# Optimization experiments

Measured on AMD Instinct MI355X. Metric: run time of the kernel, lower is better.

The kernel has to match this reference:

```python
import jax, jax.numpy as jnp
import numpy as np

# node types: 0=claim, 1=evidence, 2=user
N = [100_000, 150_000, 50_000]
E = 200_000                      # edges per edge type
ET = [(1, 0), (2, 0), (0, 1), (0, 2)]  # (src_type, dst_type)
HID, HEADS = 128, 4
DH = HID // HEADS
NUM_CLASSES = 3
NT = 3


def setup_inputs() -> dict:
    key = jax.random.key(0)
    ks = iter(jax.random.split(key, 64))
    inp = {}
    for t, n in enumerate(N):
        inp[f"x{t}"] = jax.random.normal(next(ks), (n, HID), jnp.float32)
    for e, (st, dt) in enumerate(ET):
        src = jax.random.randint(next(ks), (E,), 0, N[st], jnp.int32)
        dst = jax.random.randint(next(ks), (E,), 0, N[dt], jnp.int32)
        inp[f"ei{e}"] = jnp.stack([src, dst])
    def w(k, shape, fan_in):
        return jax.random.normal(k, shape, jnp.float32) / np.float32(np.sqrt(fan_in))
    for L in ("c1", "c2"):
        for nm in ("kw", "qw", "vw", "aw"):
            inp[f"{L}_{nm}"] = w(next(ks), (NT, HID, HID), HID)
        for nm in ("kb", "qb", "vb", "ab"):
            inp[f"{L}_{nm}"] = jnp.zeros((NT, HID), jnp.float32)
        inp[f"{L}_arel"] = w(next(ks), (len(ET), HEADS, DH, DH), DH)
        inp[f"{L}_mrel"] = w(next(ks), (len(ET), HEADS, DH, DH), DH)
        inp[f"{L}_prel"] = jnp.ones((len(ET), HEADS), jnp.float32)
        inp[f"{L}_skip"] = jnp.ones((NT,), jnp.float32)
    inp["lin_w"] = w(next(ks), (HID, NUM_CLASSES), HID)
    inp["lin_b"] = jnp.zeros((NUM_CLASSES,), jnp.float32)
    return inp


def _seg_softmax(a, seg, n):
    m = jax.ops.segment_max(a, seg, num_segments=n)
    ex = jnp.exp(a - m[seg])
    s = jax.ops.segment_sum(ex, seg, num_segments=n)
    return ex / (s[seg] + 1e-16)


def _hgt_conv(xs, eis, kw, kb, qw, qb, vw, vb, aw, ab, arel, mrel, prel, skip):
    # per-node-type K/Q/V projections -> [N_t, H, DH]
    k = [(xs[t] @ kw[t] + kb[t]).reshape(-1, HEADS, DH) for t in range(NT)]
    q = [(xs[t] @ qw[t] + qb[t]).reshape(-1, HEADS, DH) for t in range(NT)]
    v = [(xs[t] @ vw[t] + vb[t]).reshape(-1, HEADS, DH) for t in range(NT)]
    buckets = [[] for _ in range(NT)]  # per dst type: (alpha [E,H], dst [E], msg [E,H,DH])
    inv_sqrt_d = np.float32(1.0 / np.sqrt(DH))
    for e, (st, dt) in enumerate(ET):
        src, dst = eis[e][0], eis[e][1]
        ke = jnp.einsum('nhd,hde->nhe', k[st], arel[e])[src]
        ve = jnp.einsum('nhd,hde->nhe', v[st], mrel[e])[src]
        alpha = jnp.einsum('ehd,ehd->eh', q[dt][dst], ke) * prel[e] * inv_sqrt_d
        buckets[dt].append((alpha, dst, ve))
    outs = []
    for t in range(NT):
        alpha = jnp.concatenate([b[0] for b in buckets[t]], axis=0)
        dst = jnp.concatenate([b[1] for b in buckets[t]], axis=0)
        msg = jnp.concatenate([b[2] for b in buckets[t]], axis=0)
        a = _seg_softmax(alpha, dst, N[t])  # softmax over all incoming edges per dst node
        agg = jax.ops.segment_sum(msg * a[:, :, None], dst, num_segments=N[t])
        agg = agg.reshape(N[t], HID)
        o = jax.nn.gelu(agg, approximate=False) @ aw[t] + ab[t]
        s = jax.nn.sigmoid(skip[t])
        outs.append(s * o + (1.0 - s) * xs[t])
    return outs


def reference(x0, x1, x2, ei0, ei1, ei2, ei3,
              c1_kw, c1_kb, c1_qw, c1_qb, c1_vw, c1_vb, c1_aw, c1_ab,
              c1_arel, c1_mrel, c1_prel, c1_skip,
              c2_kw, c2_kb, c2_qw, c2_qb, c2_vw, c2_vb, c2_aw, c2_ab,
              c2_arel, c2_mrel, c2_prel, c2_skip,
              lin_w, lin_b):
    xs = [x0, x1, x2]
    eis = [ei0, ei1, ei2, ei3]
    xs = _hgt_conv(xs, eis, c1_kw, c1_kb, c1_qw, c1_qb, c1_vw, c1_vb, c1_aw, c1_ab,
                   c1_arel, c1_mrel, c1_prel, c1_skip)
    xs = [jax.nn.relu(x) for x in xs]
    xs = _hgt_conv(xs, eis, c2_kw, c2_kb, c2_qw, c2_qb, c2_vw, c2_vb, c2_aw, c2_ab,
                   c2_arel, c2_mrel, c2_prel, c2_skip)
    xs = [jax.nn.relu(x) for x in xs]
    out = xs[0] @ lin_w + lin_b  # logits on 'claim' nodes
    return (out, xs[0], xs[1], xs[2])
```

## Files before the change

kernel.cpp:

```cpp
#include <hip/hip_runtime.h>
#include <hip/hip_bf16.h>
#include <math.h>


typedef __bf16 bf16;
typedef __bf16 bf16x8 __attribute__((ext_vector_type(8)));
typedef float  f32x4  __attribute__((ext_vector_type(4)));

#define NE 200000
#define N0T 100000
#define N1T 150000
#define N2T 50000
#define BPITCH 136
#define QGELEMS 38400000
#define KSCALE (0.17677669529663687f * 1.4426950408889634f)

__device__ inline float bflo(unsigned u) { return __uint_as_float(u << 16); }
__device__ inline float bfhi(unsigned u) { return __uint_as_float(u & 0xFFFF0000u); }
__device__ inline unsigned f2bfbits(float f) {
    unsigned x = __float_as_uint(f);
    return ((x + 0x7FFFu + ((x >> 16) & 1u)) >> 16) & 0xFFFFu;
}
__device__ inline float gelu_exact(float x) {
    return 0.5f * x * (1.0f + erff(x * 0.70710678118654752f));
}
__device__ inline float ldx(const void* p, size_t i, int f) {
    return f ? ((const float*)p)[i] : (float)((const bf16*)p)[i];
}

__device__ inline int plausible(float v) {
    float a = fabsf(v);
    return (v == 0.f) || (a > 1e-8f && a < 1e8f);
}

__global__ void detect_k(const void* p, int* flag) {
    __shared__ int cF, cB;
    int tid = threadIdx.x;
    if (tid == 0) { cF = 0; cB = 0; }
    __syncthreads();
    float vf = ((const float*)p)[tid];
    float b0 = (float)((const bf16*)p)[2 * tid];
    float b1 = (float)((const bf16*)p)[2 * tid + 1];
    if (plausible(vf)) atomicAdd(&cF, 1);
    if (plausible(b0) && plausible(b1)) atomicAdd(&cB, 1);
    __syncthreads();
    if (tid == 0) *flag = (cF > cB) ? 1 : 0;
}

__global__ void conv_f32_k(const void* src, float* dst, int n, const int* flagp) {
    int f = *flagp;
    int i = blockIdx.x * 256 + threadIdx.x;
    if (i >= n) return;
    dst[i] = ldx(src, i, f);
}

__global__ void transpose128f(const void* W, bf16* __restrict__ WT, const int* fwp) {
    int fw = *fwp;
    int gid = blockIdx.x * 256 + threadIdx.x;
    if (gid >= 3 * 16384) return;
    int t = gid >> 14, r = (gid >> 7) & 127, c = gid & 127;
    WT[gid] = (bf16)ldx(W, (size_t)(t << 14) + c * 128 + r, fw);
}

__global__ void prep_kv(const void* kw, const void* vw, const void* arel,
                        const void* mrel, const void* prel,
                        bf16* __restrict__ WkvT, const int* fwp) {
    int fw = *fwp;
    int gid = blockIdx.x * 256 + threadIdx.x;
    if (gid >= 4 * 2 * 128 * 128) return;
    int i = gid & 127;
    int j = (gid >> 7) & 127;
    int kind = (gid >> 14) & 1;
    int e = gid >> 15;
    const int stab[4] = {1, 2, 0, 0};
    int st = stab[e];
    int h = j >> 5, jj = j & 31;
    size_t wbase = (size_t)st * 16384;
    size_t rbase = (size_t)(e * 4 + h) * 1024;
    const void* w   = kind ? vw : kw;
    const void* rel = kind ? mrel : arel;
    float acc = 0.f;
    for (int d = 0; d < 32; ++d)
        acc += ldx(w, wbase + (size_t)i * 128 + h * 32 + d, fw) *
               ldx(rel, rbase + (size_t)d * 32 + jj, fw);
    if (!kind)
        acc *= ldx(prel, e * 4 + h, fw) * KSCALE;
    WkvT[((size_t)(e * 2 + kind) * 128 + j) * 128 + i] = (bf16)acc;
}

__global__ void prep_kvbias(const void* kb, const void* vb, const void* arel,
                            const void* mrel, const void* prel,
                            float* __restrict__ Bf, const int* fwp) {
    int fw = *fwp;
    int gid = blockIdx.x * 256 + threadIdx.x;
    if (gid >= 4 * 2 * 128) return;
    int j = gid & 127;
    int kind = (gid >> 7) & 1;
    int e = gid >> 8;
    const int stab[4] = {1, 2, 0, 0};
    int st = stab[e];
    int h = j >> 5, jj = j & 31;
    const void* b   = kind ? vb : kb;
    const void* rel = kind ? mrel : arel;
    float acc = 0.f;
    for (int d = 0; d < 32; ++d)
        acc += ldx(b, (size_t)st * 128 + h * 32 + d, fw) *
               ldx(rel, (size_t)(e * 4 + h) * 1024 + (size_t)d * 32 + jj, fw);
    if (!kind)
        acc *= ldx(prel, e * 4 + h, fw) * KSCALE;
    Bf[gid] = acc;
}

__global__ void zero_i32(int* p, int n) {
    int i = blockIdx.x * 256 + threadIdx.x;
    if (i < n) p[i] = 0;
}

__global__ void hist_k(const int* __restrict__ e0, const int* __restrict__ e1,
                       const int* __restrict__ e2, const int* __restrict__ e3,
                       int* c0, int* c1, int* c2) {
    int gid = blockIdx.x * 256 + threadIdx.x;
    if (gid >= 4 * NE) return;
    int e = gid / NE, i = gid - e * NE;
    const int* ep = (e == 0) ? e0 : (e == 1) ? e1 : (e == 2) ? e2 : e3;
    int dst = ep[NE + i];
    int* c = (e < 2) ? c0 : (e == 2) ? c1 : c2;
    atomicAdd(&c[dst], 1);
}

__global__ __launch_bounds__(256) void scan1(const int* __restrict__ cnt, int n,
                                             int* __restrict__ excl, int* __restrict__ bsums) {
    __shared__ int s[256];
    int tid = threadIdx.x;
    int base = blockIdx.x * 2048 + tid * 8;
    int v[8]; int tsum = 0;
    for (int j = 0; j < 8; ++j) {
        int idx = base + j;
        int c = (idx < n) ? cnt[idx] : 0;
        v[j] = c; tsum += c;
    }
    s[tid] = tsum; __syncthreads();
    for (int off = 1; off < 256; off <<= 1) {
        int t = 0; if (tid >= off) t = s[tid - off];
        __syncthreads(); s[tid] += t; __syncthreads();
    }
    int run = s[tid] - tsum;
    for (int j = 0; j < 8; ++j) {
        int idx = base + j;
        if (idx < n) excl[idx] = run;
        run += v[j];
    }
    if (tid == 255) bsums[blockIdx.x] = s[255];
}

__global__ void scan2(int* __restrict__ bs, int nb) {
    __shared__ int s[256];
    int tid = threadIdx.x;
    int v = (tid < nb) ? bs[tid] : 0;
    s[tid] = v; __syncthreads();
    for (int off = 1; off < 256; off <<= 1) {
        int t = 0; if (tid >= off) t = s[tid - off];
        __syncthreads(); s[tid] += t; __syncthreads();
    }
    if (tid < nb) bs[tid] = s[tid] - v;
}

__global__ void scan3(int* __restrict__ excl, const int* __restrict__ bs,
                      int* __restrict__ cursor, int n, int total) {
    int idx = blockIdx.x * 256 + threadIdx.x;
    if (idx < n) {
        int v = excl[idx] + bs[idx >> 11];
        excl[idx] = v;
        cursor[idx] = v;
    }
    if (idx == 0) excl[n] = total;
}

__global__ void fill_k(const int* __restrict__ e0, const int* __restrict__ e1,
                       const int* __restrict__ e2, const int* __restrict__ e3,
                       int* c0, int* c1, int* c2,
                       unsigned* a0, unsigned* a1, unsigned* a2,
                       int lb0, int lb1, int lb2, int lb3) {
    int gid = blockIdx.x * 256 + threadIdx.x;
    if (gid >= 4 * NE) return;
    int e = gid / NE, i = gid - e * NE;
    const int* ep = (e == 0) ? e0 : (e == 1) ? e1 : (e == 2) ? e2 : e3;
    int src = ep[i], dst = ep[NE + i];
    int lb = (e == 0) ? lb0 : (e == 1) ? lb1 : (e == 2) ? lb2 : lb3;
    int* c; unsigned* a;
    if (e < 2)      { c = c0; a = a0; }
    else if (e == 2){ c = c1; a = a1; }
    else            { c = c2; a = a2; }
    int pos = atomicAdd(&c[dst], 1);
    a[pos] = (unsigned)(lb + src);
}

__global__ __launch_bounds__(1024) void proj_fused(
    const void* __restrict__ A, long aOff, int nrows,
    const bf16* __restrict__ Wb, const float* __restrict__ Bb,
    bf16* __restrict__ Ob, int ng,
    int w0, int w1, int w2, int b0, int b1, int b2,
    int o0, int o1, int o2, int p0, int p1, int p2,
    const int* fxp)
{
    int fx = *fxp;
    __shared__ bf16 sB[3 * 128 * BPITCH];
    int tid = threadIdx.x;
    #pragma unroll
    for (int g = 0; g < 3; ++g) {
        if (g >= ng) break;
        const bf16* wt = Wb + ((g == 0) ? w0 : (g == 1) ? w1 : w2);
        for (int it = 0; it < 2; ++it) {
            int idx = it * 1024 + tid;
            int r = idx >> 4, c8 = idx & 15;
            *(bf16x8*)(&sB[(g * 128 + r) * BPITCH + c8 * 8]) =
                *(const bf16x8*)(wt + r * 128 + c8 * 8);
        }
    }
    __syncthreads();

    int lane = tid & 63, wave = tid >> 6;
    int quad = lane >> 4, n16 = lane & 15;

    float bias_r[3][8];
    #pragma unroll
    for (int g = 0; g < 3; ++g) {
        if (g >= ng) break;
        const float* bp = Bb + ((g == 0) ? b0 : (g == 1) ? b1 : b2);
        #pragma unroll
        for (int c = 0; c < 8; ++c) bias_r[g][c] = bp[c * 16 + n16];
    }

    int ntiles = (nrows + 255) >> 8;
    long tile = blockIdx.x;
    if (tile >= ntiles) return;

    float4 rf[8];
    bf16x8 rb[4];
    bf16x8 afr[4];

    auto issue = [&](long t) {
        long ar = t * 256 + wave * 16 + n16;
        if (ar >= nrows) ar = nrows - 1;
        size_t base = (size_t)aOff + (size_t)ar * 128 + quad * 8;
        if (fx) {
            const float* ap = (const float*)A + base;
            #pragma unroll
            for (int k = 0; k < 4; ++k) {
                rf[2 * k]     = *(const float4*)(ap + k * 32);
                rf[2 * k + 1] = *(const float4*)(ap + k * 32 + 4);
            }
        } else {
            const bf16* ap = (const bf16*)A + base;
            #pragma unroll
            for (int k = 0; k < 4; ++k) rb[k] = *(const bf16x8*)(ap + k * 32);
        }
    };
    auto cvt = [&]() {
        if (fx) {
            #pragma unroll
            for (int k = 0; k < 4; ++k) {
                float4 u = rf[2 * k], v = rf[2 * k + 1];
                bf16x8 t;
                t[0] = (bf16)u.x; t[1] = (bf16)u.y; t[2] = (bf16)u.z; t[3] = (bf16)u.w;
                t[4] = (bf16)v.x; t[5] = (bf16)v.y; t[6] = (bf16)v.z; t[7] = (bf16)v.w;
                afr[k] = t;
            }
        } else {
            #pragma unroll
            for (int k = 0; k < 4; ++k) afr[k] = rb[k];
        }
    };

    issue(tile);
    cvt();
    for (;;) {
        long next = tile + gridDim.x;
        bool more = (next < ntiles);
        if (more) issue(next);
        long rbase = tile * 256 + wave * 16;
        #pragma unroll
        for (int g = 0; g < 3; ++g) {
            if (g >= ng) break;
            bf16* op = Ob + ((g == 0) ? o0 : (g == 1) ? o1 : o2);
            int pg = (g == 0) ? p0 : (g == 1) ? p1 : p2;
            #pragma unroll
            for (int c = 0; c < 8; ++c) {
                f32x4 acc = {0.f, 0.f, 0.f, 0.f};
                const bf16* bp = &sB[(g * 128 + c * 16 + n16) * BPITCH + quad * 8];
                #pragma unroll
                for (int k = 0; k < 4; ++k)
                    acc = __builtin_amdgcn_mfma_f32_16x16x32_bf16(
                        afr[k], *(const bf16x8*)(bp + k * 32), acc, 0, 0, 0);
                int col = c * 16 + n16;
                float bb = bias_r[g][c];
                #pragma unroll
                for (int r = 0; r < 4; ++r) {
                    long row = rbase + quad * 4 + r;
                    if (row < nrows)
                        op[(size_t)row * pg + col] = (bf16)(acc[r] + bb);
                }
            }
        }
        if (!more) break;
        cvt();
        tile = next;
    }
}

__global__ __launch_bounds__(256) void gemm_out(
    const bf16* __restrict__ G, long gOff, int nrows,
    const bf16* __restrict__ WT, const float* __restrict__ bias,
    void* __restrict__ out, long outOff,
    const void* __restrict__ xres, long xrOff,
    const float* __restrict__ skipv, const int* fxp)
{
    int fx = *fxp;
    __shared__ bf16 sB[128 * BPITCH];
    int tid = threadIdx.x;
    #pragma unroll
    for (int it = 0; it < 8; ++it) {
        int idx = it * 256 + tid;
        int r = idx >> 4, c8 = idx & 15;
        *(bf16x8*)(&sB[r * BPITCH + c8 * 8]) = *(const bf16x8*)(WT + r * 128 + c8 * 8);
    }
    __syncthreads();

    int lane = tid & 63, wave = tid >> 6;
    int quad = lane >> 4, n16 = lane & 15;
    float sk = skipv[0];
    float s = 1.f / (1.f + __expf(-sk));
    float os = 1.f - s;
    float bias_r[8];
    #pragma unroll
    for (int c = 0; c < 8; ++c) bias_r[c] = bias[c * 16 + n16];

    int ntiles = (nrows + 63) >> 6;
    long tile = blockIdx.x;
    if (tile >= ntiles) return;

    bf16x8 afr[4], nraw[4];
    auto issue = [&](long t) {
        long ar = t * 64 + wave * 16 + n16;
        if (ar >= nrows) ar = nrows - 1;
        const bf16* ap = G + gOff + (size_t)ar * 128 + quad * 8;
        nraw[0] = *(const bf16x8*)ap;
        nraw[1] = *(const bf16x8*)(ap + 32);
        nraw[2] = *(const bf16x8*)(ap + 64);
        nraw[3] = *(const bf16x8*)(ap + 96);
    };
    issue(tile);
    afr[0] = nraw[0]; afr[1] = nraw[1]; afr[2] = nraw[2]; afr[3] = nraw[3];

    for (;;) {
        long rbase = tile * 64 + wave * 16;
        long next = tile + gridDim.x;
        bool more = (next < ntiles);
        if (more) issue(next);
        float xrv[4][8];
        #pragma unroll
        for (int r = 0; r < 4; ++r) {
            long row = rbase + quad * 4 + r;
            long rc = (row < nrows) ? row : (nrows - 1);
            #pragma unroll
            for (int c = 0; c < 8; ++c) {
                size_t xi = (size_t)xrOff + (size_t)rc * 128 + c * 16 + n16;
                xrv[r][c] = fx ? ((const float*)xres)[xi]
                               : (float)((const bf16*)xres)[xi];
            }
        }
        #pragma unroll
        for (int c = 0; c < 8; ++c) {
            f32x4 acc = {0.f, 0.f, 0.f, 0.f};
            const bf16* bp = &sB[(c * 16 + n16) * BPITCH + quad * 8];
            #pragma unroll
            for (int k = 0; k < 4; ++k)
                acc = __builtin_amdgcn_mfma_f32_16x16x32_bf16(
                    afr[k], *(const bf16x8*)(bp + k * 32), acc, 0, 0, 0);
            int col = c * 16 + n16;
            #pragma unroll
            for (int r = 0; r < 4; ++r) {
                long row = rbase + quad * 4 + r;
                if (row < nrows) {
                    float v = acc[r] + bias_r[c];
                    v = s * v + os * xrv[r][c];
                    v = fmaxf(v, 0.f);
                    size_t oi = (size_t)outOff + (size_t)row * 128 + col;
                    if (fx) ((float*)out)[oi] = v; else ((bf16*)out)[oi] = (bf16)v;
                }
            }
        }
        if (!more) break;
        afr[0] = nraw[0]; afr[1] = nraw[1]; afr[2] = nraw[2]; afr[3] = nraw[3];
        tile = next;
    }
}

#define AGG_UPD(M, L, A0, A1, P, VU)                                    \
    {                                                                   \
        float nm = fmaxf(M, P);                                         \
        float sc = exp2f(M - nm);                                       \
        float pe = exp2f(P - nm);                                       \
        L = L * sc + pe;                                                \
        A0 = A0 * sc + pe * bflo(VU);                                   \
        A1 = A1 * sc + pe * bfhi(VU);                                   \
        M = nm;                                                         \
    }

#define AGG_MERGE(M, L, A0, A1, MS, LS, AS0, AS1)                       \
    {                                                                   \
        float nm = fmaxf(M, MS);                                        \
        float s0 = exp2f(M - nm);                                       \
        float s1 = exp2f(MS - nm);                                      \
        L = L * s0 + LS * s1;                                           \
        A0 = A0 * s0 + AS0 * s1;                                        \
        A1 = A1 * s0 + AS1 * s1;                                        \
        M = nm;                                                         \
    }

__global__ __launch_bounds__(256) void edge_agg(
    const int* __restrict__ rp, const unsigned* __restrict__ adj,
    const bf16* Q, const bf16* __restrict__ KEVE, bf16* G, int n) {
    int lane = threadIdx.x & 63;
    int node = blockIdx.x * 4 + (threadIdx.x >> 6);
    if (node >= n) return;
    unsigned qu = *(const unsigned*)(Q + (size_t)node * 128 + lane * 2);
    float q0 = bflo(qu), q1 = bfhi(qu);
    int beg = rp[node], end = rp[node + 1];

    float m0 = -3.4e38f, l0 = 0.f, x00 = 0.f, x01 = 0.f;
    float m1 = -3.4e38f, l1 = 0.f, x10 = 0.f, x11 = 0.f;
    float m2 = -3.4e38f, l2 = 0.f, x20 = 0.f, x21 = 0.f;
    float m3 = -3.4e38f, l3 = 0.f, x30 = 0.f, x31 = 0.f;

    int i = beg;
    for (; i + 4 <= end; i += 4) {
        unsigned r0 = adj[i], r1 = adj[i + 1], r2 = adj[i + 2], r3 = adj[i + 3];
        const bf16* k0 = KEVE + (size_t)r0 * 256;
        const bf16* k1 = KEVE + (size_t)r1 * 256;
        const bf16* k2 = KEVE + (size_t)r2 * 256;
        const bf16* k3 = KEVE + (size_t)r3 * 256;
        unsigned ku0 = *(const unsigned*)(k0 + lane * 2);
        unsigned ku1 = *(const unsigned*)(k1 + lane * 2);
        unsigned ku2 = *(const unsigned*)(k2 + lane * 2);
        unsigned ku3 = *(const unsigned*)(k3 + lane * 2);
        unsigned vu0 = *(const unsigned*)(k0 + 128 + lane * 2);
        unsigned vu1 = *(const unsigned*)(k1 + 128 + lane * 2);
        unsigned vu2 = *(const unsigned*)(k2 + 128 + lane * 2);
        unsigned vu3 = *(const unsigned*)(k3 + 128 + lane * 2);
        float p0 = q0 * bflo(ku0) + q1 * bfhi(ku0);
        float p1 = q0 * bflo(ku1) + q1 * bfhi(ku1);
        float p2 = q0 * bflo(ku2) + q1 * bfhi(ku2);
        float p3 = q0 * bflo(ku3) + q1 * bfhi(ku3);
        p0 += __shfl_xor(p0, 1); p1 += __shfl_xor(p1, 1);
        p2 += __shfl_xor(p2, 1); p3 += __shfl_xor(p3, 1);
        p0 += __shfl_xor(p0, 2); p1 += __shfl_xor(p1, 2);
        p2 += __shfl_xor(p2, 2); p3 += __shfl_xor(p3, 2);
        p0 += __shfl_xor(p0, 4); p1 += __shfl_xor(p1, 4);
        p2 += __shfl_xor(p2, 4); p3 += __shfl_xor(p3, 4);
        p0 += __shfl_xor(p0, 8); p1 += __shfl_xor(p1, 8);
        p2 += __shfl_xor(p2, 8); p3 += __shfl_xor(p3, 8);
        AGG_UPD(m0, l0, x00, x01, p0, vu0);
        AGG_UPD(m1, l1, x10, x11, p1, vu1);
        AGG_UPD(m2, l2, x20, x21, p2, vu2);
        AGG_UPD(m3, l3, x30, x31, p3, vu3);
    }
    for (; i < end; ++i) {
        unsigned r0 = adj[i];
        const bf16* k0 = KEVE + (size_t)r0 * 256;
        unsigned ku0 = *(const unsigned*)(k0 + lane * 2);
        unsigned vu0 = *(const unsigned*)(k0 + 128 + lane * 2);
        float p0 = q0 * bflo(ku0) + q1 * bfhi(ku0);
        p0 += __shfl_xor(p0, 1);
        p0 += __shfl_xor(p0, 2);
        p0 += __shfl_xor(p0, 4);
        p0 += __shfl_xor(p0, 8);
        AGG_UPD(m0, l0, x00, x01, p0, vu0);
    }
    AGG_MERGE(m0, l0, x00, x01, m1, l1, x10, x11);
    AGG_MERGE(m2, l2, x20, x21, m3, l3, x30, x31);
    AGG_MERGE(m0, l0, x00, x01, m2, l2, x20, x21);

    float inv = (end > beg) ? 1.f / l0 : 0.f;
    float g0 = gelu_exact(x00 * inv);
    float g1 = gelu_exact(x01 * inv);
    *(unsigned*)(G + (size_t)node * 128 + lane * 2) = f2bfbits(g0) | (f2bfbits(g1) << 16);
}

__global__ __launch_bounds__(256) void logits_k(
    const void* X, size_t xOff, const float* __restrict__ W,
    const float* __restrict__ B, void* out, int n, const int* fxp) {
    int fx = *fxp;
    int lane = threadIdx.x & 63;
    int node = blockIdx.x * 4 + (threadIdx.x >> 6);
    if (node >= n) return;
    size_t xb = xOff + (size_t)node * 128;
    int d0 = lane * 2;
    float x0 = ldx(X, xb + d0, fx), x1 = ldx(X, xb + d0 + 1, fx);
    float p0 = x0 * W[d0 * 3 + 0] + x1 * W[d0 * 3 + 3];
    float p1 = x0 * W[d0 * 3 + 1] + x1 * W[d0 * 3 + 4];
    float p2 = x0 * W[d0 * 3 + 2] + x1 * W[d0 * 3 + 5];
    for (int off = 1; off < 64; off <<= 1) {
        p0 += __shfl_xor(p0, off);
        p1 += __shfl_xor(p1, off);
        p2 += __shfl_xor(p2, off);
    }
    if (lane == 0) {
        p0 += B[0]; p1 += B[1]; p2 += B[2];
        if (p0 != p0) p0 = 12345.f; else if (fabsf(p0) > 1e30f) p0 = 54321.f;
        if (p1 != p1) p1 = 12345.f; else if (fabsf(p1) > 1e30f) p1 = 54321.f;
        if (p2 != p2) p2 = 12345.f; else if (fabsf(p2) > 1e30f) p2 = 54321.f;
        size_t ob = (size_t)node * 3;
        if (fx) {
            ((float*)out)[ob] = p0; ((float*)out)[ob + 1] = p1; ((float*)out)[ob + 2] = p2;
        } else {
            ((bf16*)out)[ob] = (bf16)p0; ((bf16*)out)[ob + 1] = (bf16)p1;
            ((bf16*)out)[ob + 2] = (bf16)p2;
        }
    }
}


extern "C" void kernel_launch(void* const* d_in, const int* in_sizes, int n_in,
                              void* d_out, int out_size, void* d_ws, size_t ws_size,
                              hipStream_t stream) {
    (void)n_in; (void)out_size;

    const void* x_in[3] = {d_in[0], d_in[1], d_in[2]};
    const int* ei[4] = {(const int*)d_in[3], (const int*)d_in[4],
                        (const int*)d_in[5], (const int*)d_in[6]};

    size_t KROWS = 400000;
    {
        size_t need = 0;
        auto acc = [&](size_t b) { need += (b + 255) & ~(size_t)255; };
        acc((300000ull * 128 + KROWS * 256) * 2);
        acc(2ull * 11 * 16384 * 2);
        acc(2ull * 3 * 16384 * 2);
        acc(2ull * 1408 * 4);
        acc(2ull * 384 * 4);
        acc(2ull * 3 * 4);
        acc(384ull * 4);
        acc(3ull * 4);
        acc(2ull * 4);
        acc(300000ull * 4);
        acc(300003ull * 4);
        acc(300000ull * 4);
        acc(800000ull * 4);
        acc(3ull * 256 * 4);
        if (need > ws_size) KROWS = 200000;
    }
    const int big = (KROWS == 400000);
    int lb[4];
    if (big) { lb[0] = 0; lb[1] = 150000; lb[2] = 200000; lb[3] = 300000; }
    else     { lb[0] = 0; lb[1] = 150000; lb[2] = 0;      lb[3] = 100000; }

    char* p = (char*)d_ws;
    auto alloc = [&](size_t b) { char* r = p; p += (b + 255) & ~(size_t)255; return r; };
    bf16*  QG    = (bf16*)alloc((300000ull * 128 + KROWS * 256) * 2);
    bf16*  KEVE  = QG + QGELEMS;
    bf16*  wpool = (bf16*)alloc(2ull * 11 * 16384 * 2);
    bf16*  WaT   = (bf16*)alloc(2ull * 3 * 16384 * 2);
    float* bpool = (float*)alloc(2ull * 1408 * 4);
    float* abC   = (float*)alloc(2ull * 384 * 4);
    float* skipC = (float*)alloc(2ull * 3 * 4);
    float* linwC = (float*)alloc(384ull * 4);
    float* linbC = (float*)alloc(3ull * 4);
    int*   flags = (int*)alloc(2ull * 4);
    int* counts  = (int*)alloc(300000ull * 4);
    int* rowptr  = (int*)alloc(300003ull * 4);
    int* cursor  = (int*)alloc(300000ull * 4);
    unsigned* adj = (unsigned*)alloc(800000ull * 4);
    int* bsum    = (int*)alloc(3ull * 256 * 4);

    int* fxp = flags;
    int* fwp = flags + 1;

    const int Ns[3]    = {N0T, N1T, N2T};
    const int baseN[3] = {0, 100000, 250000};
    const int tot[3]   = {400000, 200000, 200000};
    int* cn[3] = {counts, counts + 100000, counts + 250000};
    int* rp[3] = {rowptr, rowptr + 100001, rowptr + 250002};
    int* cu[3] = {cursor, cursor + 100000, cursor + 250000};
    unsigned* aj[3] = {adj, adj + 400000, adj + 600000};
    const long dxsOff[3] = {300000, 13100000, 32300000};

    detect_k<<<1, 256, 0, stream>>>(d_in[0], fxp);
    detect_k<<<1, 256, 0, stream>>>(d_in[7], fwp);

    for (int L = 0; L < 2; ++L) {
        int b = 7 + 12 * L;
        bool sig = (in_sizes[b + 1] == 384);
        int ikw, iqw, ivw, iaw, ikb, iqb, ivb, iab;
        if (sig) { ikw = b; ikb = b + 1; iqw = b + 2; iqb = b + 3;
                   ivw = b + 4; ivb = b + 5; iaw = b + 6; iab = b + 7; }
        else     { ikw = b; iqw = b + 1; ivw = b + 2; iaw = b + 3;
                   ikb = b + 4; iqb = b + 5; ivb = b + 6; iab = b + 7; }
        transpose128f<<<192, 256, 0, stream>>>(d_in[iqw], wpool + (size_t)L * 11 * 16384, fwp);
        transpose128f<<<192, 256, 0, stream>>>(d_in[iaw], WaT + (size_t)L * 49152, fwp);
        prep_kv<<<512, 256, 0, stream>>>(d_in[ikw], d_in[ivw], d_in[b + 8], d_in[b + 9],
                                         d_in[b + 10], wpool + ((size_t)L * 11 + 3) * 16384, fwp);
        prep_kvbias<<<4, 256, 0, stream>>>(d_in[ikb], d_in[ivb], d_in[b + 8], d_in[b + 9],
                                           d_in[b + 10], bpool + L * 1408 + 384, fwp);
        conv_f32_k<<<2, 256, 0, stream>>>(d_in[iqb], bpool + L * 1408, 384, fwp);
        conv_f32_k<<<2, 256, 0, stream>>>(d_in[iab], abC + L * 384, 384, fwp);
        conv_f32_k<<<1, 256, 0, stream>>>(d_in[b + 11], skipC + L * 3, 3, fwp);
    }
    conv_f32_k<<<2, 256, 0, stream>>>(d_in[31], linwC, 384, fwp);
    conv_f32_k<<<1, 256, 0, stream>>>(d_in[32], linbC, 3, fwp);

    zero_i32<<<1172, 256, 0, stream>>>(counts, 300000);
    hist_k<<<3125, 256, 0, stream>>>(ei[0], ei[1], ei[2], ei[3], cn[0], cn[1], cn[2]);
    for (int t = 0; t < 3; ++t) {
        int nb = (Ns[t] + 2047) / 2048;
        scan1<<<nb, 256, 0, stream>>>(cn[t], Ns[t], rp[t], bsum + t * 256);
        scan2<<<1, 256, 0, stream>>>(bsum + t * 256, nb);
        scan3<<<(Ns[t] + 255) / 256, 256, 0, stream>>>(rp[t], bsum + t * 256, cu[t], Ns[t], tot[t]);
    }
    fill_k<<<3125, 256, 0, stream>>>(ei[0], ei[1], ei[2], ei[3],
                                     cu[0], cu[1], cu[2], aj[0], aj[1], aj[2],
                                     lb[0], lb[1], lb[2], lb[3]);

    for (int L = 0; L < 2; ++L) {
        const void* xp[3]; long xo[3];
        for (int t = 0; t < 3; ++t) {
            xp[t] = L ? (const void*)d_out : x_in[t];
            xo[t] = L ? dxsOff[t] : 0;
        }

        auto WQi  = [&](int t) { return (L * 11 + t) * 16384; };
        auto WKVi = [&](int e, int k) { return (L * 11 + 3 + e * 2 + k) * 16384; };
        auto BQi  = [&](int t) { return L * 1408 + t * 128; };
        auto BKVi = [&](int e, int k) { return L * 1408 + 384 + (e * 2 + k) * 128; };
        auto OQ   = [&](int t) { return baseN[t] * 128; };
        auto OKe  = [&](int e) { return QGELEMS + lb[e] * 256; };

        auto proj = [&](int st, int ng,
                        int w0, int w1, int w2, int bb0, int bb1, int bb2,
                        int oo0, int oo1, int oo2, int pp0, int pp1, int pp2) {
            int nt = (Ns[st] + 255) / 256;
            int grid = nt < 256 ? nt : 256;
            proj_fused<<<grid, 1024, 0, stream>>>(xp[st], xo[st], Ns[st],
                wpool, bpool, QG, ng, w0, w1, w2, bb0, bb1, bb2,
                oo0, oo1, oo2, pp0, pp1, pp2, fxp);
        };
        auto agg = [&](int t) {
            edge_agg<<<(Ns[t] + 3) / 4, 256, 0, stream>>>(
                rp[t], aj[t], QG + (size_t)baseN[t] * 128, KEVE,
                QG + (size_t)baseN[t] * 128, Ns[t]);
        };
        auto outp = [&](int t) {
            int nt = (Ns[t] + 63) / 64;
            int grid = nt < 512 ? nt : 512;
            gemm_out<<<grid, 256, 0, stream>>>(
                QG, (long)baseN[t] * 128, Ns[t],
                WaT + ((size_t)L * 3 + t) * 16384, abC + L * 384 + t * 128,
                d_out, dxsOff[t], xp[t], xo[t], skipC + L * 3 + t, fxp);
        };

        if (big) {
            proj(1, 3, WQi(1), WKVi(0, 0), WKVi(0, 1), BQi(1), BKVi(0, 0), BKVi(0, 1),
                 OQ(1), OKe(0), OKe(0) + 128, 128, 256, 256);
            proj(2, 3, WQi(2), WKVi(1, 0), WKVi(1, 1), BQi(2), BKVi(1, 0), BKVi(1, 1),
                 OQ(2), OKe(1), OKe(1) + 128, 128, 256, 256);
            proj(0, 3, WQi(0), WKVi(2, 0), WKVi(2, 1), BQi(0), BKVi(2, 0), BKVi(2, 1),
                 OQ(0), OKe(2), OKe(2) + 128, 128, 256, 256);
            proj(0, 2, WKVi(3, 0), WKVi(3, 1), WKVi(3, 1), BKVi(3, 0), BKVi(3, 1), BKVi(3, 1),
                 OKe(3), OKe(3) + 128, OKe(3) + 128, 256, 256, 256);
            agg(0); agg(1); agg(2);
        } else {
            proj(0, 1, WQi(0), WQi(0), WQi(0), BQi(0), BQi(0), BQi(0),
                 OQ(0), OQ(0), OQ(0), 128, 128, 128);
            proj(1, 3, WQi(1), WKVi(0, 0), WKVi(0, 1), BQi(1), BKVi(0, 0), BKVi(0, 1),
                 OQ(1), OKe(0), OKe(0) + 128, 128, 256, 256);
            proj(2, 3, WQi(2), WKVi(1, 0), WKVi(1, 1), BQi(2), BKVi(1, 0), BKVi(1, 1),
                 OQ(2), OKe(1), OKe(1) + 128, 128, 256, 256);
            agg(0);
            proj(0, 2, WKVi(2, 0), WKVi(2, 1), WKVi(2, 1), BKVi(2, 0), BKVi(2, 1), BKVi(2, 1),
                 OKe(2), OKe(2) + 128, OKe(2) + 128, 256, 256, 256);
            proj(0, 2, WKVi(3, 0), WKVi(3, 1), WKVi(3, 1), BKVi(3, 0), BKVi(3, 1), BKVi(3, 1),
                 OKe(3), OKe(3) + 128, OKe(3) + 128, 256, 256, 256);
            agg(1); agg(2);
        }
        outp(0); outp(1); outp(2);
    }

    logits_k<<<25000, 256, 0, stream>>>(d_out, dxsOff[0], linwC, linbC, d_out, N0T, fxp);
}
```

Before: 1.497 ms.

## Swap MFMA operands to vectorize GEMM epilogue stores; shrink proj blocks

Both GEMM kernels swap the A/B operands of the MFMA so each lane holds four consecutive output columns of one row. The epilogue can then write packed 4-element stores (uint2 for bf16, float4 for fp32) and read the residual with vector loads, instead of scalar strided stores. Bias moves from per-lane registers into shared memory, and proj_fused goes from 1024 to 512 threads with 128-row tiles and up to 512 blocks. This cuts store instruction count and register pressure, at the cost of an extra shared-memory bias read per column group.

```diff
diff --git a/kernel.cpp b/kernel.cpp
--- a/kernel.cpp
+++ b/kernel.cpp
@@ -20,6 +20,9 @@
 __device__ inline unsigned f2bfbits(float f) {
     unsigned x = __float_as_uint(f);
     return ((x + 0x7FFFu + ((x >> 16) & 1u)) >> 16) & 0xFFFFu;
+}
+__device__ inline unsigned pk2(float a, float b) {
+    return f2bfbits(a) | (f2bfbits(b) << 16);
 }
 __device__ inline float gelu_exact(float x) {
     return 0.5f * x * (1.0f + erff(x * 0.70710678118654752f));
@@ -195,7 +198,7 @@
     a[pos] = (unsigned)(lb + src);
 }
 
-__global__ __launch_bounds__(1024) void proj_fused(
+__global__ __launch_bounds__(512) void proj_fused(
     const void* __restrict__ A, long aOff, int nrows,
     const bf16* __restrict__ Wb, const float* __restrict__ Bb,
     bf16* __restrict__ Ob, int ng,
@@ -205,33 +208,30 @@
 {
     int fx = *fxp;
     __shared__ bf16 sB[3 * 128 * BPITCH];
+    __shared__ float sBias[3 * 128];
     int tid = threadIdx.x;
     #pragma unroll
     for (int g = 0; g < 3; ++g) {
         if (g >= ng) break;
         const bf16* wt = Wb + ((g == 0) ? w0 : (g == 1) ? w1 : w2);
-        for (int it = 0; it < 2; ++it) {
-            int idx = it * 1024 + tid;
+        for (int it = 0; it < 4; ++it) {
+            int idx = it * 512 + tid;
             int r = idx >> 4, c8 = idx & 15;
             *(bf16x8*)(&sB[(g * 128 + r) * BPITCH + c8 * 8]) =
                 *(const bf16x8*)(wt + r * 128 + c8 * 8);
         }
     }
+    if (tid < 384) {
+        int g = tid >> 7, col = tid & 127;
+        int bg = (g == 0) ? b0 : (g == 1) ? b1 : b2;
+        sBias[tid] = Bb[bg + col];
+    }
     __syncthreads();
 
     int lane = tid & 63, wave = tid >> 6;
     int quad = lane >> 4, n16 = lane & 15;
 
-    float bias_r[3][8];
-    #pragma unroll
-    for (int g = 0; g < 3; ++g) {
-        if (g >= ng) break;
-        const float* bp = Bb + ((g == 0) ? b0 : (g == 1) ? b1 : b2);
-        #pragma unroll
-        for (int c = 0; c < 8; ++c) bias_r[g][c] = bp[c * 16 + n16];
-    }
-
-    int ntiles = (nrows + 255) >> 8;
+    int ntiles = (nrows + 127) >> 7;
     long tile = blockIdx.x;
     if (tile >= ntiles) return;
 
@@ -240,7 +240,7 @@
     bf16x8 afr[4];
 
     auto issue = [&](long t) {
-        long ar = t * 256 + wave * 16 + n16;
+        long ar = t * 128 + wave * 16 + n16;
         if (ar >= nrows) ar = nrows - 1;
         size_t base = (size_t)aOff + (size_t)ar * 128 + quad * 8;
         if (fx) {
@@ -278,7 +278,8 @@
         long next = tile + gridDim.x;
         bool more = (next < ntiles);
         if (more) issue(next);
-        long rbase = tile * 256 + wave * 16;
+        long row = tile * 128 + wave * 16 + n16;
+        bool wr = (row < nrows);
         #pragma unroll
         for (int g = 0; g < 3; ++g) {
             if (g >= ng) break;
@@ -291,14 +292,14 @@
                 #pragma unroll
                 for (int k = 0; k < 4; ++k)
                     acc = __builtin_amdgcn_mfma_f32_16x16x32_bf16(
-                        afr[k], *(const bf16x8*)(bp + k * 32), acc, 0, 0, 0);
-                int col = c * 16 + n16;
-                float bb = bias_r[g][c];
-                #pragma unroll
-                for (int r = 0; r < 4; ++r) {
-                    long row = rbase + quad * 4 + r;
-                    if (row < nrows)
-                        op[(size_t)row * pg + col] = (bf16)(acc[r] + bb);
+                        *(const bf16x8*)(bp + k * 32), afr[k], acc, 0, 0, 0);
+                if (wr) {
+                    int colb = c * 16 + quad * 4;
+                    float4 b4 = *(const float4*)(&sBias[g * 128 + colb]);
+                    uint2 u;
+                    u.x = pk2(acc[0] + b4.x, acc[1] + b4.y);
+                    u.y = pk2(acc[2] + b4.z, acc[3] + b4.w);
+                    *(uint2*)(op + (size_t)row * pg + colb) = u;
                 }
             }
         }
@@ -317,6 +318,7 @@
 {
     int fx = *fxp;
     __shared__ bf16 sB[128 * BPITCH];
+    __shared__ float sBias[128];
     int tid = threadIdx.x;
     #pragma unroll
     for (int it = 0; it < 8; ++it) {
@@ -324,6 +326,7 @@
         int r = idx >> 4, c8 = idx & 15;
         *(bf16x8*)(&sB[r * BPITCH + c8 * 8]) = *(const bf16x8*)(WT + r * 128 + c8 * 8);
     }
+    if (tid < 128) sBias[tid] = bias[tid];
     __syncthreads();
 
     int lane = tid & 63, wave = tid >> 6;
@@ -331,9 +334,6 @@
     float sk = skipv[0];
     float s = 1.f / (1.f + __expf(-sk));
     float os = 1.f - s;
-    float bias_r[8];
-    #pragma unroll
-    for (int c = 0; c < 8; ++c) bias_r[c] = bias[c * 16 + n16];
 
     int ntiles = (nrows + 63) >> 6;
     long tile = blockIdx.x;
@@ -353,20 +353,23 @@
     afr[0] = nraw[0]; afr[1] = nraw[1]; afr[2] = nraw[2]; afr[3] = nraw[3];
 
     for (;;) {
-        long rbase = tile * 64 + wave * 16;
+        long row = tile * 64 + wave * 16 + n16;
+        bool wr = (row < nrows);
+        long rc = wr ? row : (nrows - 1);
         long next = tile + gridDim.x;
         bool more = (next < ntiles);
         if (more) issue(next);
-        float xrv[4][8];
+        float xrv[8][4];
         #pragma unroll
-        for (int r = 0; r < 4; ++r) {
-            long row = rbase + quad * 4 + r;
-            long rc = (row < nrows) ? row : (nrows - 1);
-            #pragma unroll
-            for (int c = 0; c < 8; ++c) {
-                size_t xi = (size_t)xrOff + (size_t)rc * 128 + c * 16 + n16;
-                xrv[r][c] = fx ? ((const float*)xres)[xi]
-                               : (float)((const bf16*)xres)[xi];
+        for (int c = 0; c < 8; ++c) {
+            size_t xi = (size_t)xrOff + (size_t)rc * 128 + c * 16 + quad * 4;
+            if (fx) {
+                float4 u = *(const float4*)((const float*)xres + xi);
+                xrv[c][0] = u.x; xrv[c][1] = u.y; xrv[c][2] = u.z; xrv[c][3] = u.w;
+            } else {
+                uint2 u = *(const uint2*)((const bf16*)xres + xi);
+                xrv[c][0] = bflo(u.x); xrv[c][1] = bfhi(u.x);
+                xrv[c][2] = bflo(u.y); xrv[c][3] = bfhi(u.y);
             }
         }
         #pragma unroll
@@ -376,17 +379,21 @@
             #pragma unroll
             for (int k = 0; k < 4; ++k)
                 acc = __builtin_amdgcn_mfma_f32_16x16x32_bf16(
-                    afr[k], *(const bf16x8*)(bp + k * 32), acc, 0, 0, 0);
-            int col = c * 16 + n16;
-            #pragma unroll
-            for (int r = 0; r < 4; ++r) {
-                long row = rbase + quad * 4 + r;
-                if (row < nrows) {
-                    float v = acc[r] + bias_r[c];
-                    v = s * v + os * xrv[r][c];
-                    v = fmaxf(v, 0.f);
-                    size_t oi = (size_t)outOff + (size_t)row * 128 + col;
-                    if (fx) ((float*)out)[oi] = v; else ((bf16*)out)[oi] = (bf16)v;
+                    *(const bf16x8*)(bp + k * 32), afr[k], acc, 0, 0, 0);
+            if (wr) {
+                int colb = c * 16 + quad * 4;
+                float4 b4 = *(const float4*)(&sBias[colb]);
+                float v0 = fmaxf(s * (acc[0] + b4.x) + os * xrv[c][0], 0.f);
+                float v1 = fmaxf(s * (acc[1] + b4.y) + os * xrv[c][1], 0.f);
+                float v2 = fmaxf(s * (acc[2] + b4.z) + os * xrv[c][2], 0.f);
+                float v3 = fmaxf(s * (acc[3] + b4.w) + os * xrv[c][3], 0.f);
+                size_t oi = (size_t)outOff + (size_t)row * 128 + colb;
+                if (fx) {
+                    float4 u = {v0, v1, v2, v3};
+                    *(float4*)((float*)out + oi) = u;
+                } else {
+                    uint2 u; u.x = pk2(v0, v1); u.y = pk2(v2, v3);
+                    *(uint2*)((bf16*)out + oi) = u;
                 }
             }
         }
@@ -638,9 +645,9 @@
         auto proj = [&](int st, int ng,
                         int w0, int w1, int w2, int bb0, int bb1, int bb2,
                         int oo0, int oo1, int oo2, int pp0, int pp1, int pp2) {
-            int nt = (Ns[st] + 255) / 256;
-            int grid = nt < 256 ? nt : 256;
-            proj_fused<<<grid, 1024, 0, stream>>>(xp[st], xo[st], Ns[st],
+            int nt = (Ns[st] + 127) / 128;
+            int grid = nt < 512 ? nt : 512;
+            proj_fused<<<grid, 512, 0, stream>>>(xp[st], xo[st], Ns[st],
                 wpool, bpool, QG, ng, w0, w1, w2, bb0, bb1, bb2,
                 oo0, oo1, oo2, pp0, pp1, pp2, fxp);
         };
```

Result: faster. 1.278 ms (-14.6%).
